# Kernel tuning notes

Measured on AMD Instinct MI355X. Metric: run time of the kernel, lower is better.

## Reference

```python
import jax, jax.numpy as jnp
import numpy as np

N = 50000   # nodes
E = 800000  # edges (avg degree 16)
H = 8       # num_heads
D = 16      # head_dim = hidden_size // num_heads = 128 // 8


def setup_inputs() -> dict:
    key = jax.random.key(0)
    k1, k2, k3, k4, k5 = jax.random.split(key, 5)
    q = jax.random.normal(k1, (N, D, H), dtype=jnp.float32)
    k = jax.random.normal(k2, (N, D, H), dtype=jnp.float32)
    v = jax.random.normal(k3, (N, D, H), dtype=jnp.float32)
    # COO adjacency: row = destination node of each edge, col = source node
    row = jnp.sort(jax.random.randint(k4, (E,), 0, N, dtype=jnp.int32))
    col = jax.random.randint(k5, (E,), 0, N, dtype=jnp.int32)
    return {"q": q, "k": k, "v": v, "row": row, "col": col}


def reference(q, k, v, row, col):
    # bsddmm: sampled dense-dense matmul -> per-edge, per-head attention logits
    # logits[e, h] = sum_d q[row[e], d, h] * k[col[e], d, h]
    logits = jnp.einsum('edh,edh->eh', q[row], k[col])  # [E, H]

    # sparse softmax over each destination row (per head), numerically stable
    m = jax.ops.segment_max(logits, row, num_segments=N)  # [N, H]
    p = jnp.exp(logits - m[row])                          # [E, H]
    s = jax.ops.segment_sum(p, row, num_segments=N)       # [N, H]
    attn = p / s[row]                                     # [E, H]

    # bspmm: out[i, d, h] = sum_{e: row[e]==i} attn[e, h] * v[col[e], d, h]
    out = jax.ops.segment_sum(attn[:, None, :] * v[col], row, num_segments=N)  # [N, D, H]
    return out.reshape(N, -1)  # [N, D*H]
```

## Files before the change

### kernel.cpp

```cpp
#include <hip/hip_runtime.h>
#include <math.h>

#define HEADS 8
#define DIM 16
#define NPB 16

static __device__ __forceinline__ unsigned short f2bf(float f) {
  unsigned u = __float_as_uint(f);
  u += 0x7FFFu + ((u >> 16) & 1u);
  return (unsigned short)(u >> 16);
}
static __device__ __forceinline__ float bflo(unsigned u) { return __uint_as_float(u << 16); }
static __device__ __forceinline__ float bfhi(unsigned u) { return __uint_as_float(u & 0xFFFF0000u); }

__global__ __launch_bounds__(256) void conv_kernel(
    const float* __restrict__ k, const float* __restrict__ v,
    unsigned short* __restrict__ kv, int N) {
  int j = blockIdx.x * blockDim.x + threadIdx.x;
  if (j >= N * 32) return;
  int i = j >> 5, c = j & 31;
  const float* src = (c < 16 ? k : v) + (size_t)i * 128 + (c & 15) * 8;
  float4 f0 = ((const float4*)src)[0];
  float4 f1 = ((const float4*)src)[1];
  uint4 r;
  r.x = (unsigned)f2bf(f0.x) | ((unsigned)f2bf(f0.y) << 16);
  r.y = (unsigned)f2bf(f0.z) | ((unsigned)f2bf(f0.w) << 16);
  r.z = (unsigned)f2bf(f1.x) | ((unsigned)f2bf(f1.y) << 16);
  r.w = (unsigned)f2bf(f1.z) | ((unsigned)f2bf(f1.w) << 16);
  *(uint4*)(kv + (size_t)i * 256 + c * 8) = r;
}

__global__ __launch_bounds__(256) void spmha_bf16_kernel(
    const float* __restrict__ q, const unsigned short* __restrict__ kv,
    const int* __restrict__ row, const int* __restrict__ col,
    float* __restrict__ out, int N, int E) {
  __shared__ int rp[NPB + 1];
  int node0 = blockIdx.x * NPB;
  if (threadIdx.x <= NPB) {
    int target = node0 + threadIdx.x;
    int lo = 0, hi = E;
    while (lo < hi) {
      int mid = (lo + hi) >> 1;
      if (row[mid] < target) lo = mid + 1; else hi = mid;
    }
    rp[threadIdx.x] = lo;
  }
  __syncthreads();

  int g  = threadIdx.x >> 3;
  int il = g >> 1;
  int sl = g & 1;
  int i  = node0 + il;
  int l  = threadIdx.x & 7;
  bool alive = (i < N);
  int s = alive ? rp[il] : 0;
  int e = alive ? rp[il + 1] : 0;

  float qv0[8], qv1[8];
  if (alive) {
    const float4* qp = (const float4*)(q + (size_t)i * 128);
    *(float4*)&qv0[0] = qp[2 * l];
    *(float4*)&qv0[4] = qp[2 * l + 1];
    *(float4*)&qv1[0] = qp[16 + 2 * l];
    *(float4*)&qv1[4] = qp[16 + 2 * l + 1];
  }

  float o0[8], o1[8], m[8], den[8];
#pragma unroll
  for (int h = 0; h < 8; ++h) { o0[h] = 0.f; o1[h] = 0.f; m[h] = -INFINITY; den[h] = 0.f; }

  auto cvt8 = [](const uint4& A, float* f) {
    f[0] = bflo(A.x); f[1] = bfhi(A.x); f[2] = bflo(A.y); f[3] = bfhi(A.y);
    f[4] = bflo(A.z); f[5] = bfhi(A.z); f[6] = bflo(A.w); f[7] = bfhi(A.w);
  };

  auto do_edge = [&](const uint4& A, const uint4& B, const uint4& C, const uint4& D) {
    float kf0[8], kf1[8], vf0[8], vf1[8];
    cvt8(A, kf0); cvt8(B, kf1); cvt8(C, vf0); cvt8(D, vf1);
    float part[8];
#pragma unroll
    for (int h = 0; h < 8; ++h) part[h] = fmaf(qv0[h], kf0[h], qv1[h] * kf1[h]);
#pragma unroll
    for (int h = 0; h < 8; ++h) part[h] += __shfl_xor(part[h], 1);
#pragma unroll
    for (int h = 0; h < 8; ++h) part[h] += __shfl_xor(part[h], 2);
#pragma unroll
    for (int h = 0; h < 8; ++h) part[h] += __shfl_xor(part[h], 4);
#pragma unroll
    for (int h = 0; h < 8; ++h) {
      float mn = fmaxf(m[h], part[h]);
      float sc = __expf(m[h] - mn);
      float p  = __expf(part[h] - mn);
      den[h] = fmaf(den[h], sc, p);
      m[h] = mn;
      o0[h] = fmaf(o0[h], sc, p * vf0[h]);
      o1[h] = fmaf(o1[h], sc, p * vf1[h]);
    }
  };

  int eidx = s + sl;
  for (; eidx + 2 < e; eidx += 4) {
    int c0 = col[eidx];
    int c1 = col[eidx + 2];
    const uint4* b0 = (const uint4*)(kv + (size_t)c0 * 256);
    const uint4* b1 = (const uint4*)(kv + (size_t)c1 * 256);
    uint4 A0 = b0[l], B0 = b0[8 + l], C0 = b0[16 + l], D0 = b0[24 + l];
    uint4 A1 = b1[l], B1 = b1[8 + l], C1 = b1[16 + l], D1 = b1[24 + l];
    do_edge(A0, B0, C0, D0);
    do_edge(A1, B1, C1, D1);
  }
  if (eidx < e) {
    int c0 = col[eidx];
    const uint4* b0 = (const uint4*)(kv + (size_t)c0 * 256);
    do_edge(b0[l], b0[8 + l], b0[16 + l], b0[24 + l]);
  }

#pragma unroll
  for (int h = 0; h < 8; ++h) {
    float m_o   = __shfl_xor(m[h], 8);
    float den_o = __shfl_xor(den[h], 8);
    float o0_o  = __shfl_xor(o0[h], 8);
    float o1_o  = __shfl_xor(o1[h], 8);
    float mn = fmaxf(m[h], m_o);
    float a  = __expf(m[h] - mn);
    float b  = __expf(m_o - mn);
    den[h] = den[h] * a + den_o * b;
    o0[h]  = o0[h] * a + o0_o * b;
    o1[h]  = o1[h] * a + o1_o * b;
  }

  if (alive && sl == 0) {
    float4* op = (float4*)(out + (size_t)i * 128);
    if (e > s) {
      float inv[8];
#pragma unroll
      for (int h = 0; h < 8; ++h) inv[h] = 1.f / den[h];
      float4 r;
      r.x = o0[0] * inv[0]; r.y = o0[1] * inv[1]; r.z = o0[2] * inv[2]; r.w = o0[3] * inv[3];
      op[2 * l] = r;
      r.x = o0[4] * inv[4]; r.y = o0[5] * inv[5]; r.z = o0[6] * inv[6]; r.w = o0[7] * inv[7];
      op[2 * l + 1] = r;
      r.x = o1[0] * inv[0]; r.y = o1[1] * inv[1]; r.z = o1[2] * inv[2]; r.w = o1[3] * inv[3];
      op[16 + 2 * l] = r;
      r.x = o1[4] * inv[4]; r.y = o1[5] * inv[5]; r.z = o1[6] * inv[6]; r.w = o1[7] * inv[7];
      op[16 + 2 * l + 1] = r;
    } else {
      float4 z = make_float4(0.f, 0.f, 0.f, 0.f);
      op[2 * l] = z; op[2 * l + 1] = z; op[16 + 2 * l] = z; op[16 + 2 * l + 1] = z;
    }
  }
}

__global__ __launch_bounds__(256) void spmha_f32_kernel(
    const float* __restrict__ q, const float* __restrict__ k, const float* __restrict__ v,
    const int* __restrict__ row, const int* __restrict__ col,
    float* __restrict__ out, int N, int E) {
  __shared__ int rp[33];
  int node0 = blockIdx.x * 32;
  if (threadIdx.x <= 32) {
    int target = node0 + threadIdx.x;
    int lo = 0, hi = E;
    while (lo < hi) {
      int mid = (lo + hi) >> 1;
      if (row[mid] < target) lo = mid + 1; else hi = mid;
    }
    rp[threadIdx.x] = lo;
  }
  __syncthreads();

  int il = threadIdx.x >> 3;
  int i  = node0 + il;
  int l  = threadIdx.x & 7;
  bool alive = (i < N);
  int s = alive ? rp[il] : 0;
  int e = alive ? rp[il + 1] : 0;

  float qv[16];
  if (alive) {
    const float4* qb = (const float4*)(q + (size_t)i * 128);
#pragma unroll
    for (int r = 0; r < 4; ++r) *(float4*)&qv[4 * r] = qb[8 * r + l];
  }
  float o[16];
#pragma unroll
  for (int x = 0; x < 16; ++x) o[x] = 0.f;
  float m[4], den[4];
#pragma unroll
  for (int j = 0; j < 4; ++j) { m[j] = -INFINITY; den[j] = 0.f; }

  auto do_edge = [&](const float* kk, const float* vv) {
    float part[4];
#pragma unroll
    for (int j = 0; j < 4; ++j) part[j] = 0.f;
#pragma unroll
    for (int r = 0; r < 4; ++r)
#pragma unroll
      for (int j = 0; j < 4; ++j)
        part[j] = fmaf(qv[4 * r + j], kk[4 * r + j], part[j]);
#pragma unroll
    for (int j = 0; j < 4; ++j) {
      part[j] += __shfl_xor(part[j], 2);
      part[j] += __shfl_xor(part[j], 4);
    }
#pragma unroll
    for (int j = 0; j < 4; ++j) {
      float mn = fmaxf(m[j], part[j]);
      float sc = __expf(m[j] - mn);
      float p  = __expf(part[j] - mn);
      den[j] = fmaf(den[j], sc, p);
      m[j] = mn;
#pragma unroll
      for (int r = 0; r < 4; ++r)
        o[4 * r + j] = fmaf(o[4 * r + j], sc, p * vv[4 * r + j]);
    }
  };

  for (int eidx = s; eidx < e; ++eidx) {
    int c0 = col[eidx];
    const float4* kb0 = (const float4*)(k + (size_t)c0 * 128);
    const float4* vb0 = (const float4*)(v + (size_t)c0 * 128);
    float kk0[16], vv0[16];
#pragma unroll
    for (int r = 0; r < 4; ++r) {
      *(float4*)&kk0[4 * r] = kb0[8 * r + l];
      *(float4*)&vv0[4 * r] = vb0[8 * r + l];
    }
    do_edge(kk0, vv0);
  }

  if (alive) {
    float inv[4];
#pragma unroll
    for (int j = 0; j < 4; ++j) inv[j] = (e > s) ? 1.f / den[j] : 0.f;
    float4* ob = (float4*)(out + (size_t)i * 128);
#pragma unroll
    for (int r = 0; r < 4; ++r) {
      float4 res;
      res.x = o[4 * r + 0] * inv[0];
      res.y = o[4 * r + 1] * inv[1];
      res.z = o[4 * r + 2] * inv[2];
      res.w = o[4 * r + 3] * inv[3];
      ob[8 * r + l] = res;
    }
  }
}

extern "C" void kernel_launch(void* const* d_in, const int* in_sizes, int n_in,
                              void* d_out, int out_size, void* d_ws, size_t ws_size,
                              hipStream_t stream) {
  const float* q   = (const float*)d_in[0];
  const float* k   = (const float*)d_in[1];
  const float* v   = (const float*)d_in[2];
  const int*   row = (const int*)d_in[3];
  const int*   col = (const int*)d_in[4];
  float* out = (float*)d_out;

  int N = in_sizes[0] / (DIM * HEADS);
  int E = in_sizes[3];

  size_t kv_bytes = (size_t)N * 512;

  if (ws_size >= kv_bytes) {
    unsigned short* kv = (unsigned short*)d_ws;
    int cgrid = (N * 32 + 255) / 256;
    conv_kernel<<<cgrid, 256, 0, stream>>>(k, v, kv, N);
    int grid = (N + NPB - 1) / NPB;
    spmha_bf16_kernel<<<grid, 256, 0, stream>>>(q, kv, row, col, out, N, E);
  } else {
    int total = N * HEADS;
    int grid = (total + 255) / 256;
    spmha_f32_kernel<<<grid, 256, 0, stream>>>(q, k, v, row, col, out, N, E);
  }
}
```

Before: 218.6 us.

## Sort nodes by degree for load balancing and deepen edge-load batching

Adds a preprocessing pipeline (CSR bounds via binary search, a degree histogram, a descending scan and a scatter) that builds a permutation ordering nodes by degree. The attention kernel then processes nodes in that order, so the nodes handled by one block have similar edge counts and warp divergence is reduced. The edge loop now issues four gathers per iteration instead of two to expose more memory-level parallelism. In exchange there are four extra small launches, including a single-thread scan, plus atomics, and output and q accesses become scattered.

```diff
diff --git a/kernel.cpp b/kernel.cpp
--- a/kernel.cpp
+++ b/kernel.cpp
@@ -30,35 +30,79 @@
   *(uint4*)(kv + (size_t)i * 256 + c * 8) = r;
 }
 
+__global__ __launch_bounds__(256) void bounds_kernel(
+    const int* __restrict__ row, int* __restrict__ bounds, int* __restrict__ hist,
+    int N, int E) {
+  if (blockIdx.x == 0 && threadIdx.x < 256) hist[threadIdx.x] = 0;
+  int t = blockIdx.x * blockDim.x + threadIdx.x;
+  if (t > N) return;
+  int lo = 0, hi = E;
+  while (lo < hi) {
+    int mid = (lo + hi) >> 1;
+    if (row[mid] < t) lo = mid + 1; else hi = mid;
+  }
+  bounds[t] = lo;
+}
+
+__global__ __launch_bounds__(256) void hist_kernel(
+    const int* __restrict__ bounds, int* __restrict__ hist, int N) {
+  int i = blockIdx.x * blockDim.x + threadIdx.x;
+  if (i >= N) return;
+  int deg = bounds[i + 1] - bounds[i];
+  atomicAdd(&hist[min(deg, 255)], 1);
+}
+
+__global__ void scan_kernel(int* __restrict__ hist) {
+  int run = 0;
+  for (int b = 255; b >= 0; --b) { int h = hist[b]; hist[b] = run; run += h; }
+}
+
+__global__ __launch_bounds__(256) void scatter_kernel(
+    const int* __restrict__ bounds, int* __restrict__ hist, int* __restrict__ perm, int N) {
+  int i = blockIdx.x * blockDim.x + threadIdx.x;
+  if (i >= N) return;
+  int deg = bounds[i + 1] - bounds[i];
+  int pos = atomicAdd(&hist[min(deg, 255)], 1);
+  perm[pos] = i;
+}
+
 __global__ __launch_bounds__(256) void spmha_bf16_kernel(
     const float* __restrict__ q, const unsigned short* __restrict__ kv,
     const int* __restrict__ row, const int* __restrict__ col,
+    const int* __restrict__ bounds, const int* __restrict__ perm,
     float* __restrict__ out, int N, int E) {
   __shared__ int rp[NPB + 1];
   int node0 = blockIdx.x * NPB;
-  if (threadIdx.x <= NPB) {
-    int target = node0 + threadIdx.x;
-    int lo = 0, hi = E;
-    while (lo < hi) {
-      int mid = (lo + hi) >> 1;
-      if (row[mid] < target) lo = mid + 1; else hi = mid;
-    }
-    rp[threadIdx.x] = lo;
-  }
-  __syncthreads();
+  if (bounds == nullptr) {
+    if (threadIdx.x <= NPB) {
+      int target = node0 + threadIdx.x;
+      int lo = 0, hi = E;
+      while (lo < hi) {
+        int mid = (lo + hi) >> 1;
+        if (row[mid] < target) lo = mid + 1; else hi = mid;
+      }
+      rp[threadIdx.x] = lo;
+    }
+    __syncthreads();
+  }
 
   int g  = threadIdx.x >> 3;
   int il = g >> 1;
   int sl = g & 1;
-  int i  = node0 + il;
   int l  = threadIdx.x & 7;
-  bool alive = (i < N);
-  int s = alive ? rp[il] : 0;
-  int e = alive ? rp[il + 1] : 0;
+  int idx = node0 + il;
+  bool alive = (idx < N);
+  int node = idx;
+  int s = 0, e = 0;
+  if (alive) {
+    if (perm) node = perm[idx];
+    if (bounds) { s = bounds[node]; e = bounds[node + 1]; }
+    else        { s = rp[il];       e = rp[il + 1]; }
+  }
 
   float qv0[8], qv1[8];
   if (alive) {
-    const float4* qp = (const float4*)(q + (size_t)i * 128);
+    const float4* qp = (const float4*)(q + (size_t)node * 128);
     *(float4*)&qv0[0] = qp[2 * l];
     *(float4*)&qv0[4] = qp[2 * l + 1];
     *(float4*)&qv1[0] = qp[16 + 2 * l];
@@ -99,20 +143,23 @@
   };
 
   int eidx = s + sl;
-  for (; eidx + 2 < e; eidx += 4) {
-    int c0 = col[eidx];
-    int c1 = col[eidx + 2];
-    const uint4* b0 = (const uint4*)(kv + (size_t)c0 * 256);
-    const uint4* b1 = (const uint4*)(kv + (size_t)c1 * 256);
-    uint4 A0 = b0[l], B0 = b0[8 + l], C0 = b0[16 + l], D0 = b0[24 + l];
-    uint4 A1 = b1[l], B1 = b1[8 + l], C1 = b1[16 + l], D1 = b1[24 + l];
-    do_edge(A0, B0, C0, D0);
-    do_edge(A1, B1, C1, D1);
-  }
-  if (eidx < e) {
-    int c0 = col[eidx];
-    const uint4* b0 = (const uint4*)(kv + (size_t)c0 * 256);
-    do_edge(b0[l], b0[8 + l], b0[16 + l], b0[24 + l]);
+  while (eidx + 6 < e) {
+    uint4 A[4], B[4], C[4], D[4];
+#pragma unroll
+    for (int j = 0; j < 4; ++j) {
+      int c = col[eidx + 2 * j];
+      const uint4* b = (const uint4*)(kv + (size_t)c * 256);
+      A[j] = b[l]; B[j] = b[8 + l]; C[j] = b[16 + l]; D[j] = b[24 + l];
+    }
+#pragma unroll
+    for (int j = 0; j < 4; ++j) do_edge(A[j], B[j], C[j], D[j]);
+    eidx += 8;
+  }
+  while (eidx < e) {
+    int c = col[eidx];
+    const uint4* b = (const uint4*)(kv + (size_t)c * 256);
+    do_edge(b[l], b[8 + l], b[16 + l], b[24 + l]);
+    eidx += 2;
   }
 
 #pragma unroll
@@ -130,7 +177,7 @@
   }
 
   if (alive && sl == 0) {
-    float4* op = (float4*)(out + (size_t)i * 128);
+    float4* op = (float4*)(out + (size_t)node * 128);
     if (e > s) {
       float inv[8];
 #pragma unroll
@@ -167,14 +214,10 @@
     rp[threadIdx.x] = lo;
   }
   __syncthreads();
-
-  int il = threadIdx.x >> 3;
-  int i  = node0 + il;
-  int l  = threadIdx.x & 7;
+  int il = threadIdx.x >> 3, i = node0 + il, l = threadIdx.x & 7;
   bool alive = (i < N);
   int s = alive ? rp[il] : 0;
   int e = alive ? rp[il + 1] : 0;
-
   float qv[16];
   if (alive) {
     const float4* qb = (const float4*)(q + (size_t)i * 128);
@@ -187,8 +230,16 @@
   float m[4], den[4];
 #pragma unroll
   for (int j = 0; j < 4; ++j) { m[j] = -INFINITY; den[j] = 0.f; }
-
-  auto do_edge = [&](const float* kk, const float* vv) {
+  for (int eidx = s; eidx < e; ++eidx) {
+    int c0 = col[eidx];
+    const float4* kb0 = (const float4*)(k + (size_t)c0 * 128);
+    const float4* vb0 = (const float4*)(v + (size_t)c0 * 128);
+    float kk0[16], vv0[16];
+#pragma unroll
+    for (int r = 0; r < 4; ++r) {
+      *(float4*)&kk0[4 * r] = kb0[8 * r + l];
+      *(float4*)&vv0[4 * r] = vb0[8 * r + l];
+    }
     float part[4];
 #pragma unroll
     for (int j = 0; j < 4; ++j) part[j] = 0.f;
@@ -196,7 +247,7 @@
     for (int r = 0; r < 4; ++r)
 #pragma unroll
       for (int j = 0; j < 4; ++j)
-        part[j] = fmaf(qv[4 * r + j], kk[4 * r + j], part[j]);
+        part[j] = fmaf(qv[4 * r + j], kk0[4 * r + j], part[j]);
 #pragma unroll
     for (int j = 0; j < 4; ++j) {
       part[j] += __shfl_xor(part[j], 2);
@@ -211,23 +262,9 @@
       m[j] = mn;
 #pragma unroll
       for (int r = 0; r < 4; ++r)
-        o[4 * r + j] = fmaf(o[4 * r + j], sc, p * vv[4 * r + j]);
-    }
-  };
-
-  for (int eidx = s; eidx < e; ++eidx) {
-    int c0 = col[eidx];
-    const float4* kb0 = (const float4*)(k + (size_t)c0 * 128);
-    const float4* vb0 = (const float4*)(v + (size_t)c0 * 128);
-    float kk0[16], vv0[16];
-#pragma unroll
-    for (int r = 0; r < 4; ++r) {
-      *(float4*)&kk0[4 * r] = kb0[8 * r + l];
-      *(float4*)&vv0[4 * r] = vb0[8 * r + l];
-    }
-    do_edge(kk0, vv0);
-  }
-
+        o[4 * r + j] = fmaf(o[4 * r + j], sc, p * vv0[4 * r + j]);
+    }
+  }
   if (alive) {
     float inv[4];
 #pragma unroll
@@ -258,17 +295,27 @@
   int N = in_sizes[0] / (DIM * HEADS);
   int E = in_sizes[3];
 
-  size_t kv_bytes = (size_t)N * 512;
-
-  if (ws_size >= kv_bytes) {
+  size_t kvB  = (size_t)N * 512;
+  size_t need = kvB + ((size_t)N + 1) * 4 + 1024 + (size_t)N * 4;
+  int grid = (N + NPB - 1) / NPB;
+
+  if (ws_size >= need) {
     unsigned short* kv = (unsigned short*)d_ws;
-    int cgrid = (N * 32 + 255) / 256;
-    conv_kernel<<<cgrid, 256, 0, stream>>>(k, v, kv, N);
-    int grid = (N + NPB - 1) / NPB;
-    spmha_bf16_kernel<<<grid, 256, 0, stream>>>(q, kv, row, col, out, N, E);
+    int* bounds = (int*)((char*)d_ws + kvB);
+    int* hist   = bounds + (N + 1);
+    int* perm   = hist + 256;
+    conv_kernel<<<(N * 32 + 255) / 256, 256, 0, stream>>>(k, v, kv, N);
+    bounds_kernel<<<(N + 1 + 255) / 256, 256, 0, stream>>>(row, bounds, hist, N, E);
+    hist_kernel<<<(N + 255) / 256, 256, 0, stream>>>(bounds, hist, N);
+    scan_kernel<<<1, 1, 0, stream>>>(hist);
+    scatter_kernel<<<(N + 255) / 256, 256, 0, stream>>>(bounds, hist, perm, N);
+    spmha_bf16_kernel<<<grid, 256, 0, stream>>>(q, kv, row, col, bounds, perm, out, N, E);
+  } else if (ws_size >= kvB) {
+    unsigned short* kv = (unsigned short*)d_ws;
+    conv_kernel<<<(N * 32 + 255) / 256, 256, 0, stream>>>(k, v, kv, N);
+    spmha_bf16_kernel<<<grid, 256, 0, stream>>>(q, kv, row, col, nullptr, nullptr, out, N, E);
   } else {
     int total = N * HEADS;
-    int grid = (total + 255) / 256;
-    spmha_f32_kernel<<<grid, 256, 0, stream>>>(q, k, v, row, col, out, N, E);
-  }
-}
+    spmha_f32_kernel<<<(total + 255) / 256, 256, 0, stream>>>(q, k, v, row, col, out, N, E);
+  }
+}
```

After: 456.0 us. 2.09x slower.
